# Kernel tuning notes

Hardware: AMD Instinct MI355X
Metric: run time of the kernel (lower is better)

## Reference

```python
import jax, jax.numpy as jnp
import numpy as np

B, S, D, DO, L, E = 8, 2048, 256, 256, 8, 32768


def setup_inputs() -> dict:
    key = jax.random.key(0)
    k1, k2, k3, k4, k5, k6 = jax.random.split(key, 6)
    node_repr = jax.random.normal(k1, (B, S, D), dtype=jnp.float32)
    edge_src = jax.random.randint(k2, (B, E), 0, S, dtype=jnp.int32)
    edge_tgt = jax.random.randint(k3, (B, E), 0, S, dtype=jnp.int32)
    edge_label = jax.random.randint(k4, (B, E), 0, L, dtype=jnp.int32)
    # per-label Linear params (torch default: kaiming-ish uniform; values here are random stand-ins)
    bound = 1.0 / np.sqrt(D)
    W = jax.random.uniform(k5, (L, D, DO), dtype=jnp.float32, minval=-bound, maxval=bound)
    b = jax.random.uniform(k6, (L, DO), dtype=jnp.float32, minval=-bound, maxval=bound)
    return {"node_repr": node_repr, "edge_src": edge_src, "edge_tgt": edge_tgt,
            "edge_label": edge_label, "W": W, "b": b}


def reference(node_repr, edge_src, edge_tgt, edge_label, W, b):
    # Transform every node by every label's linear once: y[b,l,s,:] = x[b,s,:] @ W[l] + b[l]
    y = jnp.einsum('bsd,ldo->blso', node_repr, W) + b[None, :, None, :]  # [B,L,S,DO]
    bidx = jnp.arange(node_repr.shape[0])[:, None]                       # [B,1]
    msgs = y[bidx, edge_label, edge_src]                                 # [B,E,DO] gather
    out = jnp.zeros(node_repr.shape[:2] + (W.shape[-1],), dtype=node_repr.dtype)
    out = out.at[bidx, edge_tgt].add(msgs)                               # scatter-add into targets
    return jax.nn.relu(out)
```

## Files before the change

### kernel.cpp

```cpp
#include <hip/hip_runtime.h>
#include <stdint.h>

constexpr int NB = 8;
constexpr int NS = 2048;
constexpr int ND = 256;
constexpr int NDO = 256;
constexpr int NL = 8;
constexpr int NE = 32768;

typedef __attribute__((ext_vector_type(8))) short bf16x8;
typedef __attribute__((ext_vector_type(4))) float f32x4;
typedef unsigned int u32;

__device__ __forceinline__ float bf2f(uint32_t u) {
    return __uint_as_float(u << 16);
}
__device__ __forceinline__ uint16_t f2bf(float f) {
    uint32_t x = __float_as_uint(f);
    uint32_t r = (x + 0x7fffu + ((x >> 16) & 1u)) >> 16;
    return (uint16_t)r;
}

__device__ __forceinline__ void gl_lds16(const void* gptr, void* lptr) {
    __builtin_amdgcn_global_load_lds(
        (const __attribute__((address_space(1))) u32*)gptr,
        (__attribute__((address_space(3))) u32*)lptr, 16, 0, 0);
}

__global__ void convert_x_kernel(const float* __restrict__ x, ushort* __restrict__ xb) {
    int i = blockIdx.x * blockDim.x + threadIdx.x;
    const float4* xv = (const float4*)x;
    float4 v = xv[i];
    ushort4 o;
    o.x = f2bf(v.x); o.y = f2bf(v.y); o.z = f2bf(v.z); o.w = f2bf(v.w);
    ((ushort4*)xb)[i] = o;
}

__global__ void convert_wt_kernel(const float* __restrict__ W, ushort* __restrict__ wt) {
    int i = blockIdx.x * blockDim.x + threadIdx.x;
    int d = i & (ND - 1);
    int o = (i >> 8) & (NDO - 1);
    int l = i >> 16;
    wt[i] = f2bf(W[(size_t)(l * ND + d) * NDO + o]);
}

__global__ void hist_kernel(const int* __restrict__ tgt, int* __restrict__ counts) {
    int i = blockIdx.x * blockDim.x + threadIdx.x;
    int b = i >> 15;
    atomicAdd(&counts[b * NS + tgt[i]], 1);
}

__global__ void scan_kernel(const int* __restrict__ counts,
                            int* __restrict__ offsets, int* __restrict__ cursor) {
    int b = blockIdx.x;
    int t = threadIdx.x;
    __shared__ int part[256];
    int base = b * NS + t * 8;
    int s = 0;
    for (int i = 0; i < 8; i++) s += counts[base + i];
    part[t] = s;
    __syncthreads();
    if (t == 0) {
        int run = 0;
        for (int i = 0; i < 256; i++) { int v = part[i]; part[i] = run; run += v; }
    }
    __syncthreads();
    int run = part[t];
    for (int i = 0; i < 8; i++) {
        offsets[base + i] = run;
        cursor[base + i] = run;
        run += counts[base + i];
    }
}

__global__ void place_kernel(const int* __restrict__ tgt,
                             const int* __restrict__ esrc, const int* __restrict__ elab,
                             int* __restrict__ cursor, int* __restrict__ sorted) {
    int i = blockIdx.x * blockDim.x + threadIdx.x;
    int b = i >> 15;
    int tg = tgt[i];
    int lab = elab[i];
    int src = esrc[i];
    int p = atomicAdd(&cursor[b * NS + tg], 1);
    sorted[b * NE + p] = (b * NL + lab) * NS + src;
}

__global__ __launch_bounds__(256) void gemm_kernel(
    const ushort* __restrict__ xb, const ushort* __restrict__ wt,
    const float* __restrict__ bias, ushort* __restrict__ y) {
    int n0 = blockIdx.x * 128;
    int m0 = blockIdx.y * 128;
    int bl = blockIdx.z;
    int b = bl >> 3;
    int l = bl & 7;

    __shared__ ushort As[128 * 32];
    __shared__ ushort Bs[128 * 32];

    int tid = threadIdx.x;
    int lane = tid & 63;
    int wave = __builtin_amdgcn_readfirstlane(tid >> 6);
    int wm = wave & 1, wn = wave >> 1;
    int ln = lane & 15, quad = lane >> 4;

    f32x4 acc[4][4] = {};

    const ushort* Ag = xb + (size_t)(b * NS + m0) * ND;
    const ushort* Bg = wt + (size_t)(l * NDO + n0) * ND;

    int r0 = tid >> 2, c0 = (tid & 3) << 3;
    int r1 = (256 + tid) >> 2, c1 = c0;

    for (int k0 = 0; k0 < ND; k0 += 32) {
        ushort* lA0 = &As[(wave * 64) * 8];
        ushort* lA1 = &As[(256 + wave * 64) * 8];
        ushort* lB0 = &Bs[(wave * 64) * 8];
        ushort* lB1 = &Bs[(256 + wave * 64) * 8];
        gl_lds16(Ag + (size_t)r0 * ND + k0 + c0, lA0);
        gl_lds16(Ag + (size_t)r1 * ND + k0 + c1, lA1);
        gl_lds16(Bg + (size_t)r0 * ND + k0 + c0, lB0);
        gl_lds16(Bg + (size_t)r1 * ND + k0 + c1, lB1);
        __syncthreads();

        bf16x8 af[4], bfr[4];
        for (int i = 0; i < 4; i++)
            af[i] = *(const bf16x8*)&As[(wm * 64 + i * 16 + ln) * 32 + quad * 8];
        for (int j = 0; j < 4; j++)
            bfr[j] = *(const bf16x8*)&Bs[(wn * 64 + j * 16 + ln) * 32 + quad * 8];
        for (int i = 0; i < 4; i++)
            for (int j = 0; j < 4; j++)
                acc[i][j] = __builtin_amdgcn_mfma_f32_16x16x32_bf16(af[i], bfr[j], acc[i][j], 0, 0, 0);
        __syncthreads();
    }

    ushort* yb = y + (size_t)(b * NL + l) * NS * NDO;
    for (int j = 0; j < 4; j++) {
        int col = n0 + wn * 64 + j * 16 + ln;
        float bv = bias[l * NDO + col];
        for (int i = 0; i < 4; i++) {
            int rbase = m0 + wm * 64 + i * 16 + quad * 4;
            for (int r = 0; r < 4; r++) {
                yb[(size_t)(rbase + r) * NDO + col] = f2bf(acc[i][j][r] + bv);
            }
        }
    }
}

__device__ __forceinline__ void accum4(float4& a, uint2 v) {
    a.x += bf2f(v.x & 0xffffu);
    a.y += bf2f(v.x >> 16);
    a.z += bf2f(v.y & 0xffffu);
    a.w += bf2f(v.y >> 16);
}

__global__ __launch_bounds__(256) void gather_kernel(
    const ushort* __restrict__ y,
    const int* __restrict__ counts, const int* __restrict__ offsets,
    const int* __restrict__ sorted, float* __restrict__ out) {
    int g = blockIdx.x * 4 + (threadIdx.x >> 6);
    int lane = threadIdx.x & 63;
    int b = g >> 11;
    int t = g & (NS - 1);

    int n = counts[b * NS + t];
    int off = offsets[b * NS + t];
    const int* ridx = sorted + (size_t)b * NE + off;

    float4 a0 = {0.f, 0.f, 0.f, 0.f};
    float4 a1 = {0.f, 0.f, 0.f, 0.f};
    float4 a2 = {0.f, 0.f, 0.f, 0.f};
    float4 a3 = {0.f, 0.f, 0.f, 0.f};

    for (int base = 0; base < n; base += 64) {
        int m = n - base;
        if (m > 64) m = 64;
        int my = (lane < m) ? ridx[base + lane] : 0;
        int k = 0;
        for (; k + 4 <= m; k += 4) {
            int i0 = __shfl(my, k);
            int i1 = __shfl(my, k + 1);
            int i2 = __shfl(my, k + 2);
            int i3 = __shfl(my, k + 3);
            uint2 v0 = ((const uint2*)(y + (size_t)i0 * NDO))[lane];
            uint2 v1 = ((const uint2*)(y + (size_t)i1 * NDO))[lane];
            uint2 v2 = ((const uint2*)(y + (size_t)i2 * NDO))[lane];
            uint2 v3 = ((const uint2*)(y + (size_t)i3 * NDO))[lane];
            accum4(a0, v0);
            accum4(a1, v1);
            accum4(a2, v2);
            accum4(a3, v3);
        }
        for (; k < m; k++) {
            int i0 = __shfl(my, k);
            uint2 v0 = ((const uint2*)(y + (size_t)i0 * NDO))[lane];
            accum4(a0, v0);
        }
    }

    float4 r;
    r.x = fmaxf(a0.x + a1.x + a2.x + a3.x, 0.f);
    r.y = fmaxf(a0.y + a1.y + a2.y + a3.y, 0.f);
    r.z = fmaxf(a0.z + a1.z + a2.z + a3.z, 0.f);
    r.w = fmaxf(a0.w + a1.w + a2.w + a3.w, 0.f);
    ((float4*)(out + (size_t)(b * NS + t) * NDO))[lane] = r;
}

extern "C" void kernel_launch(void* const* d_in, const int* in_sizes, int n_in,
                              void* d_out, int out_size, void* d_ws, size_t ws_size,
                              hipStream_t stream) {
    const float* x    = (const float*)d_in[0];
    const int*   esrc = (const int*)d_in[1];
    const int*   etgt = (const int*)d_in[2];
    const int*   elab = (const int*)d_in[3];
    const float* W    = (const float*)d_in[4];
    const float* bias = (const float*)d_in[5];
    float* out = (float*)d_out;

    char* ws = (char*)d_ws;
    ushort* xb     = (ushort*)(ws);
    ushort* wt     = (ushort*)(ws + 8388608);
    ushort* y      = (ushort*)(ws + 9437184);
    int*    counts = (int*)(ws + 76546048);
    int*    offs   = (int*)(ws + 76611584);
    int*    cursor = (int*)(ws + 76677120);
    int*    sorted = (int*)(ws + 76742656);

    hipMemsetAsync(counts, 0, NB * NS * sizeof(int), stream);

    convert_x_kernel<<<4096, 256, 0, stream>>>(x, xb);
    convert_wt_kernel<<<2048, 256, 0, stream>>>(W, wt);
    hist_kernel<<<1024, 256, 0, stream>>>(etgt, counts);
    scan_kernel<<<NB, 256, 0, stream>>>(counts, offs, cursor);
    place_kernel<<<1024, 256, 0, stream>>>(etgt, esrc, elab, cursor, sorted);
    gemm_kernel<<<dim3(2, 16, 64), 256, 0, stream>>>(xb, wt, bias, y);
    gather_kernel<<<4096, 256, 0, stream>>>(y, counts, offs, sorted, out);
}
```

Before: 167.9 us.

## Aggregate node features per target and label before a single stacked GEMM

Reorders the computation so edges are bucketed by (target, label) and raw node features are summed per bucket into a [B*S, L*D] matrix. A single GEMM with K=L*D against the stacked weights then produces the output, with the count-weighted bias sum and ReLU fused into its epilogue. This removes the per-label transformed tensor y and its bf16 gather, but it adds a large intermediate Z that must be written and reread. The bias sum is stored in bf16, and the GEMM uses smaller tiles over a long K loop.

```diff
diff --git a/kernel.cpp b/kernel.cpp
--- a/kernel.cpp
+++ b/kernel.cpp
@@ -7,6 +7,7 @@
 constexpr int NDO = 256;
 constexpr int NL = 8;
 constexpr int NE = 32768;
+constexpr int K2 = NL * ND;
 
 typedef __attribute__((ext_vector_type(8))) short bf16x8;
 typedef __attribute__((ext_vector_type(4))) float f32x4;
@@ -27,37 +28,28 @@
         (__attribute__((address_space(3))) u32*)lptr, 16, 0, 0);
 }
 
-__global__ void convert_x_kernel(const float* __restrict__ x, ushort* __restrict__ xb) {
-    int i = blockIdx.x * blockDim.x + threadIdx.x;
-    const float4* xv = (const float4*)x;
-    float4 v = xv[i];
-    ushort4 o;
-    o.x = f2bf(v.x); o.y = f2bf(v.y); o.z = f2bf(v.z); o.w = f2bf(v.w);
-    ((ushort4*)xb)[i] = o;
-}
-
-__global__ void convert_wt_kernel(const float* __restrict__ W, ushort* __restrict__ wt) {
-    int i = blockIdx.x * blockDim.x + threadIdx.x;
-    int d = i & (ND - 1);
-    int o = (i >> 8) & (NDO - 1);
-    int l = i >> 16;
-    wt[i] = f2bf(W[(size_t)(l * ND + d) * NDO + o]);
-}
-
-__global__ void hist_kernel(const int* __restrict__ tgt, int* __restrict__ counts) {
+__global__ void convert_wt2_kernel(const float* __restrict__ W, ushort* __restrict__ wt2) {
+    int j = blockIdx.x * blockDim.x + threadIdx.x;
+    int k = j & (K2 - 1);
+    int o = j >> 11;
+    wt2[j] = f2bf(W[(size_t)k * NDO + o]);
+}
+
+__global__ void hist2_kernel(const int* __restrict__ tgt, const int* __restrict__ lab,
+                             int* __restrict__ counts) {
     int i = blockIdx.x * blockDim.x + threadIdx.x;
     int b = i >> 15;
-    atomicAdd(&counts[b * NS + tgt[i]], 1);
-}
-
-__global__ void scan_kernel(const int* __restrict__ counts,
-                            int* __restrict__ offsets, int* __restrict__ cursor) {
+    atomicAdd(&counts[(b << 14) + tgt[i] * NL + lab[i]], 1);
+}
+
+__global__ void scan2_kernel(const int* __restrict__ counts,
+                             int* __restrict__ offsets, int* __restrict__ cursor) {
     int b = blockIdx.x;
     int t = threadIdx.x;
     __shared__ int part[256];
-    int base = b * NS + t * 8;
+    int base = (b << 14) + t * 64;
     int s = 0;
-    for (int i = 0; i < 8; i++) s += counts[base + i];
+    for (int i = 0; i < 64; i++) s += counts[base + i];
     part[t] = s;
     __syncthreads();
     if (t == 0) {
@@ -66,35 +58,92 @@
     }
     __syncthreads();
     int run = part[t];
-    for (int i = 0; i < 8; i++) {
+    for (int i = 0; i < 64; i++) {
         offsets[base + i] = run;
         cursor[base + i] = run;
         run += counts[base + i];
     }
 }
 
-__global__ void place_kernel(const int* __restrict__ tgt,
-                             const int* __restrict__ esrc, const int* __restrict__ elab,
-                             int* __restrict__ cursor, int* __restrict__ sorted) {
+__global__ void place2_kernel(const int* __restrict__ tgt,
+                              const int* __restrict__ esrc, const int* __restrict__ elab,
+                              int* __restrict__ cursor, int* __restrict__ sorted) {
     int i = blockIdx.x * blockDim.x + threadIdx.x;
     int b = i >> 15;
-    int tg = tgt[i];
-    int lab = elab[i];
-    int src = esrc[i];
-    int p = atomicAdd(&cursor[b * NS + tg], 1);
-    sorted[b * NE + p] = (b * NL + lab) * NS + src;
-}
-
-__global__ __launch_bounds__(256) void gemm_kernel(
-    const ushort* __restrict__ xb, const ushort* __restrict__ wt,
-    const float* __restrict__ bias, ushort* __restrict__ y) {
-    int n0 = blockIdx.x * 128;
-    int m0 = blockIdx.y * 128;
-    int bl = blockIdx.z;
-    int b = bl >> 3;
-    int l = bl & 7;
-
-    __shared__ ushort As[128 * 32];
+    int p = atomicAdd(&cursor[(b << 14) + tgt[i] * NL + elab[i]], 1);
+    sorted[(b << 15) + p] = esrc[i];
+}
+
+__global__ __launch_bounds__(256) void agg_kernel(
+    const float* __restrict__ x, const float* __restrict__ bias,
+    const int* __restrict__ offs, const int* __restrict__ sorted,
+    ushort* __restrict__ Z, ushort* __restrict__ bsum) {
+    int g = blockIdx.x * 4 + (threadIdx.x >> 6);
+    int lane = threadIdx.x & 63;
+    int b = g >> 11;
+    int t = g & (NS - 1);
+
+    int off = offs[g << 3];
+    int end = (t == NS - 1) ? NE : offs[(g + 1) << 3];
+    int ov = (lane < 8) ? offs[(g << 3) + lane] : end;
+    int n = end - off;
+
+    const int* ep = sorted + ((size_t)b << 15) + off;
+    const float4* x4 = (const float4*)x + (size_t)b * NS * 64;
+    ushort* zrow = Z + (size_t)g * K2;
+
+    float4 a; a.x = a.y = a.z = a.w = 0.f;
+    int cur = 0;
+    int onext = __shfl(ov, 1);
+    int p = off;
+    for (int base = 0; base < n; base += 64) {
+        int m = n - base;
+        if (m > 64) m = 64;
+        int my = (lane < m) ? ep[base + lane] : 0;
+        for (int k = 0; k < m; k++) {
+            while (p >= onext) {
+                ushort4 ob;
+                ob.x = f2bf(a.x); ob.y = f2bf(a.y); ob.z = f2bf(a.z); ob.w = f2bf(a.w);
+                ((ushort4*)(zrow + cur * ND))[lane] = ob;
+                a.x = a.y = a.z = a.w = 0.f;
+                cur++;
+                onext = __shfl(ov, cur + 1);
+            }
+            int src = __shfl(my, k);
+            float4 xv = x4[src * 64 + lane];
+            a.x += xv.x; a.y += xv.y; a.z += xv.z; a.w += xv.w;
+            p++;
+        }
+    }
+    for (; cur < 8; cur++) {
+        ushort4 ob;
+        ob.x = f2bf(a.x); ob.y = f2bf(a.y); ob.z = f2bf(a.z); ob.w = f2bf(a.w);
+        ((ushort4*)(zrow + cur * ND))[lane] = ob;
+        a.x = a.y = a.z = a.w = 0.f;
+    }
+
+    float4 ab; ab.x = ab.y = ab.z = ab.w = 0.f;
+#pragma unroll
+    for (int l = 0; l < 8; l++) {
+        int c0 = __shfl(ov, l);
+        int c1 = __shfl(ov, l + 1);
+        float cf = (float)(c1 - c0);
+        float4 bv = ((const float4*)bias)[l * 64 + lane];
+        ab.x += cf * bv.x; ab.y += cf * bv.y; ab.z += cf * bv.z; ab.w += cf * bv.w;
+    }
+    ushort4 sb;
+    sb.x = f2bf(ab.x); sb.y = f2bf(ab.y); sb.z = f2bf(ab.z); sb.w = f2bf(ab.w);
+    ((ushort4*)(bsum + (size_t)g * NDO))[lane] = sb;
+}
+
+__global__ __launch_bounds__(256) void gemm2_kernel(
+    const ushort* __restrict__ Z, const ushort* __restrict__ wt2,
+    const ushort* __restrict__ bsum, float* __restrict__ out) {
+    int wgid = (blockIdx.x & 7) * 64 + (blockIdx.x >> 3);
+    int m0 = (wgid >> 1) * 64;
+    int n0 = (wgid & 1) * 128;
+
+    __shared__ ushort As[64 * 32];
     __shared__ ushort Bs[128 * 32];
 
     int tid = threadIdx.x;
@@ -103,106 +152,41 @@
     int wm = wave & 1, wn = wave >> 1;
     int ln = lane & 15, quad = lane >> 4;
 
-    f32x4 acc[4][4] = {};
-
-    const ushort* Ag = xb + (size_t)(b * NS + m0) * ND;
-    const ushort* Bg = wt + (size_t)(l * NDO + n0) * ND;
+    f32x4 acc[2][4] = {};
+
+    const ushort* Ag = Z + (size_t)m0 * K2;
+    const ushort* Bg = wt2 + (size_t)n0 * K2;
 
     int r0 = tid >> 2, c0 = (tid & 3) << 3;
-    int r1 = (256 + tid) >> 2, c1 = c0;
-
-    for (int k0 = 0; k0 < ND; k0 += 32) {
-        ushort* lA0 = &As[(wave * 64) * 8];
-        ushort* lA1 = &As[(256 + wave * 64) * 8];
-        ushort* lB0 = &Bs[(wave * 64) * 8];
-        ushort* lB1 = &Bs[(256 + wave * 64) * 8];
-        gl_lds16(Ag + (size_t)r0 * ND + k0 + c0, lA0);
-        gl_lds16(Ag + (size_t)r1 * ND + k0 + c1, lA1);
-        gl_lds16(Bg + (size_t)r0 * ND + k0 + c0, lB0);
-        gl_lds16(Bg + (size_t)r1 * ND + k0 + c1, lB1);
+
+    for (int k0 = 0; k0 < K2; k0 += 32) {
+        gl_lds16(Ag + (size_t)r0 * K2 + k0 + c0, &As[wave * 512]);
+        gl_lds16(Bg + (size_t)r0 * K2 + k0 + c0, &Bs[wave * 512]);
+        gl_lds16(Bg + (size_t)(64 + r0) * K2 + k0 + c0, &Bs[2048 + wave * 512]);
         __syncthreads();
 
-        bf16x8 af[4], bfr[4];
-        for (int i = 0; i < 4; i++)
-            af[i] = *(const bf16x8*)&As[(wm * 64 + i * 16 + ln) * 32 + quad * 8];
+        bf16x8 af[2], bfr[4];
+        for (int i = 0; i < 2; i++)
+            af[i] = *(const bf16x8*)&As[(wm * 32 + i * 16 + ln) * 32 + quad * 8];
         for (int j = 0; j < 4; j++)
             bfr[j] = *(const bf16x8*)&Bs[(wn * 64 + j * 16 + ln) * 32 + quad * 8];
-        for (int i = 0; i < 4; i++)
+        for (int i = 0; i < 2; i++)
             for (int j = 0; j < 4; j++)
                 acc[i][j] = __builtin_amdgcn_mfma_f32_16x16x32_bf16(af[i], bfr[j], acc[i][j], 0, 0, 0);
         __syncthreads();
     }
 
-    ushort* yb = y + (size_t)(b * NL + l) * NS * NDO;
     for (int j = 0; j < 4; j++) {
         int col = n0 + wn * 64 + j * 16 + ln;
-        float bv = bias[l * NDO + col];
-        for (int i = 0; i < 4; i++) {
-            int rbase = m0 + wm * 64 + i * 16 + quad * 4;
+        for (int i = 0; i < 2; i++) {
+            int rbase = m0 + wm * 32 + i * 16 + quad * 4;
             for (int r = 0; r < 4; r++) {
-                yb[(size_t)(rbase + r) * NDO + col] = f2bf(acc[i][j][r] + bv);
+                size_t idx = (size_t)(rbase + r) * NDO + col;
+                float v = acc[i][j][r] + bf2f(bsum[idx]);
+                out[idx] = fmaxf(v, 0.f);
             }
         }
     }
-}
-
-__device__ __forceinline__ void accum4(float4& a, uint2 v) {
-    a.x += bf2f(v.x & 0xffffu);
-    a.y += bf2f(v.x >> 16);
-    a.z += bf2f(v.y & 0xffffu);
-    a.w += bf2f(v.y >> 16);
-}
-
-__global__ __launch_bounds__(256) void gather_kernel(
-    const ushort* __restrict__ y,
-    const int* __restrict__ counts, const int* __restrict__ offsets,
-    const int* __restrict__ sorted, float* __restrict__ out) {
-    int g = blockIdx.x * 4 + (threadIdx.x >> 6);
-    int lane = threadIdx.x & 63;
-    int b = g >> 11;
-    int t = g & (NS - 1);
-
-    int n = counts[b * NS + t];
-    int off = offsets[b * NS + t];
-    const int* ridx = sorted + (size_t)b * NE + off;
-
-    float4 a0 = {0.f, 0.f, 0.f, 0.f};
-    float4 a1 = {0.f, 0.f, 0.f, 0.f};
-    float4 a2 = {0.f, 0.f, 0.f, 0.f};
-    float4 a3 = {0.f, 0.f, 0.f, 0.f};
-
-    for (int base = 0; base < n; base += 64) {
-        int m = n - base;
-        if (m > 64) m = 64;
-        int my = (lane < m) ? ridx[base + lane] : 0;
-        int k = 0;
-        for (; k + 4 <= m; k += 4) {
-            int i0 = __shfl(my, k);
-            int i1 = __shfl(my, k + 1);
-            int i2 = __shfl(my, k + 2);
-            int i3 = __shfl(my, k + 3);
-            uint2 v0 = ((const uint2*)(y + (size_t)i0 * NDO))[lane];
-            uint2 v1 = ((const uint2*)(y + (size_t)i1 * NDO))[lane];
-            uint2 v2 = ((const uint2*)(y + (size_t)i2 * NDO))[lane];
-            uint2 v3 = ((const uint2*)(y + (size_t)i3 * NDO))[lane];
-            accum4(a0, v0);
-            accum4(a1, v1);
-            accum4(a2, v2);
-            accum4(a3, v3);
-        }
-        for (; k < m; k++) {
-            int i0 = __shfl(my, k);
-            uint2 v0 = ((const uint2*)(y + (size_t)i0 * NDO))[lane];
-            accum4(a0, v0);
-        }
-    }
-
-    float4 r;
-    r.x = fmaxf(a0.x + a1.x + a2.x + a3.x, 0.f);
-    r.y = fmaxf(a0.y + a1.y + a2.y + a3.y, 0.f);
-    r.z = fmaxf(a0.z + a1.z + a2.z + a3.z, 0.f);
-    r.w = fmaxf(a0.w + a1.w + a2.w + a3.w, 0.f);
-    ((float4*)(out + (size_t)(b * NS + t) * NDO))[lane] = r;
 }
 
 extern "C" void kernel_launch(void* const* d_in, const int* in_sizes, int n_in,
@@ -217,21 +201,20 @@
     float* out = (float*)d_out;
 
     char* ws = (char*)d_ws;
-    ushort* xb     = (ushort*)(ws);
-    ushort* wt     = (ushort*)(ws + 8388608);
-    ushort* y      = (ushort*)(ws + 9437184);
+    ushort* wt2    = (ushort*)(ws);
+    ushort* Z      = (ushort*)(ws + 1048576);
+    ushort* bsum   = (ushort*)(ws + 68157440);
     int*    counts = (int*)(ws + 76546048);
-    int*    offs   = (int*)(ws + 76611584);
-    int*    cursor = (int*)(ws + 76677120);
-    int*    sorted = (int*)(ws + 76742656);
-
-    hipMemsetAsync(counts, 0, NB * NS * sizeof(int), stream);
-
-    convert_x_kernel<<<4096, 256, 0, stream>>>(x, xb);
-    convert_wt_kernel<<<2048, 256, 0, stream>>>(W, wt);
-    hist_kernel<<<1024, 256, 0, stream>>>(etgt, counts);
-    scan_kernel<<<NB, 256, 0, stream>>>(counts, offs, cursor);
-    place_kernel<<<1024, 256, 0, stream>>>(etgt, esrc, elab, cursor, sorted);
-    gemm_kernel<<<dim3(2, 16, 64), 256, 0, stream>>>(xb, wt, bias, y);
-    gather_kernel<<<4096, 256, 0, stream>>>(y, counts, offs, sorted, out);
-}
+    int*    offs   = (int*)(ws + 78643200);
+    int*    cursor = (int*)(ws + 80740352);
+    int*    sorted = (int*)(ws + 82837504);
+
+    hipMemsetAsync(counts, 0, NB * NS * NL * sizeof(int), stream);
+
+    convert_wt2_kernel<<<2048, 256, 0, stream>>>(W, wt2);
+    hist2_kernel<<<1024, 256, 0, stream>>>(etgt, elab, counts);
+    scan2_kernel<<<NB, 256, 0, stream>>>(counts, offs, cursor);
+    place2_kernel<<<1024, 256, 0, stream>>>(etgt, esrc, elab, cursor, sorted);
+    agg_kernel<<<4096, 256, 0, stream>>>(x, bias, offs, sorted, Z, bsum);
+    gemm2_kernel<<<512, 256, 0, stream>>>(Z, wt2, bsum, out);
+}
```

New measurement: 185.1 us. 10.3% more time.
